# Kernel tuning notes

Measured on AMD Instinct MI355X. Metric: run time of the kernel, lower is better.

## Reference

```python
import jax, jax.numpy as jnp
import numpy as np

N_SAMPLE, N_RES = 1024, 4096

def setup_inputs() -> dict:
    key = jax.random.key(0)
    k1, k2 = jax.random.split(key)
    pred = jax.random.normal(k1, (N_SAMPLE, N_RES, 3), dtype=jnp.float32)
    true = jax.random.normal(k2, (N_RES, 3), dtype=jnp.float32)
    mask = jnp.ones((N_RES,), dtype=jnp.bool_)
    return {"pred_coordinate": pred, "true_coordinate": true, "coordinate_mask": mask}


def _tm_score(pred_coordinate, true_coordinate, coordinate_mask):
    # mask used as weights: identical to torch's boolean gather + reduce
    w = coordinate_mask.astype(jnp.float32)           # [L]
    Lt = jnp.sum(w)                                   # number of valid residues
    # d0 normalization (RNA uses protein formula), clamped at 0.5
    d0 = jnp.where(Lt <= 15.0, 0.5, 1.24 * jnp.cbrt(Lt - 15.0) - 1.8)
    d0 = jnp.maximum(d0, 0.5)
    d0_sq = d0 * d0

    wn = w / Lt                                       # normalized weights [L]
    true_mean = jnp.einsum('l,li->i', wn, true_coordinate)              # [3]
    pred_mean = jnp.einsum('l,sli->si', wn, pred_coordinate)            # [S,3]
    pred_c = pred_coordinate - pred_mean[:, None, :]                    # [S,L,3]
    true_c = true_coordinate - true_mean                                # [L,3]

    # Kabsch: covariance H_s = pred_c^T diag(w) true_c  -> [S,3,3]
    H = jnp.einsum('sli,l,lj->sij', pred_c, w, true_c)
    U, _, Vt = jnp.linalg.svd(H, full_matrices=False)
    V = jnp.swapaxes(Vt, -1, -2)
    # proper rotation (no reflection): flip sign of last singular vector if det<0
    det = jnp.linalg.det(jnp.einsum('sij,skj->sik', V, U))              # det(V U^T)
    D = jnp.stack([jnp.ones_like(det), jnp.ones_like(det), jnp.sign(det)], axis=-1)  # [S,3]
    R = jnp.einsum('sij,sj,skj->sik', V, D, U)        # R = V diag(D) U^T, [S,3,3]

    aligned = jnp.einsum('sij,slj->sli', R, pred_c) + true_mean         # [S,L,3]
    d_sq = jnp.sum((aligned - true_coordinate) ** 2, axis=-1)           # [S,L]
    terms = 1.0 / (1.0 + d_sq / d0_sq)
    tm = jnp.einsum('sl,l->s', terms, wn)             # masked mean -> [S]
    return tm


def reference(pred_coordinate, true_coordinate, coordinate_mask):
    return _tm_score(pred_coordinate, true_coordinate, coordinate_mask)
```

## Files before the change

### kernel.cpp

```cpp
#include <hip/hip_runtime.h>
#include <math.h>


#define NS        1024
#define NL        4096
#define TPB       256
#define CHUNK_RES 1024
#define NCHUNK    4

__device__ __forceinline__ float waveReduceSum(float v) {
    #pragma unroll
    for (int off = 32; off > 0; off >>= 1)
        v += __shfl_down(v, off, 64);
    return v;
}

__device__ __forceinline__ double det3(const double B[4][4],
                                       int r0, int r1, int r2,
                                       int c0, int c1, int c2) {
    return B[r0][c0]*(B[r1][c1]*B[r2][c2] - B[r1][c2]*B[r2][c1])
         - B[r0][c1]*(B[r1][c0]*B[r2][c2] - B[r1][c2]*B[r2][c0])
         + B[r0][c2]*(B[r1][c0]*B[r2][c1] - B[r1][c1]*B[r2][c0]);
}

__global__ __launch_bounds__(TPB, 4) void tm_fused(
    const float* __restrict__ pred, const float* __restrict__ tru,
    const int* __restrict__ mask, float* __restrict__ out)
{
    const int s    = blockIdx.x;
    const int tid  = threadIdx.x;
    const int wave = tid >> 6, lane = tid & 63;
    const float* ps = pred + (size_t)s * NL * 3;

    __shared__ float ldsP[CHUNK_RES * 3];
    __shared__ float ldsT[CHUNK_RES * 3];
    __shared__ float sred[4][18];

    float acc[18];
    #pragma unroll
    for (int i = 0; i < 18; ++i) acc[i] = 0.f;

    for (int k = 0; k < NCHUNK; ++k) {
        const float4* gp = (const float4*)(ps  + (size_t)k * CHUNK_RES * 3);
        const float4* gt = (const float4*)(tru + (size_t)k * CHUNK_RES * 3);
        float4* lp = (float4*)ldsP;
        float4* lt = (float4*)ldsT;
        #pragma unroll
        for (int j = 0; j < 3; ++j) {
            const int idx = wave * 192 + j * 64 + lane;
            lp[idx] = gp[idx];
            lt[idx] = gt[idx];
        }
        __syncthreads();

        const float4* rp = (const float4*)&ldsP[tid * 12];
        const float4* rt = (const float4*)&ldsT[tid * 12];
        const float4 q0 = rp[0], q1 = rp[1], q2 = rp[2];
        const float4 u0 = rt[0], u1 = rt[1], u2 = rt[2];
        const int4   mi = *(const int4*)(mask + k * CHUNK_RES + tid * 4);

        const float px[4] = {q0.x, q0.w, q1.z, q2.y};
        const float py[4] = {q0.y, q1.x, q1.w, q2.z};
        const float pz[4] = {q0.z, q1.y, q2.x, q2.w};
        const float tx[4] = {u0.x, u0.w, u1.z, u2.y};
        const float ty[4] = {u0.y, u1.x, u1.w, u2.z};
        const float tz[4] = {u0.z, u1.y, u2.x, u2.w};
        const float wm[4] = {mi.x ? 1.f : 0.f, mi.y ? 1.f : 0.f,
                             mi.z ? 1.f : 0.f, mi.w ? 1.f : 0.f};

        #pragma unroll
        for (int r = 0; r < 4; ++r) {
            const float w = wm[r];
            const float wpx = w * px[r], wpy = w * py[r], wpz = w * pz[r];
            acc[0] += w;
            acc[1] += w * tx[r]; acc[2] += w * ty[r]; acc[3] += w * tz[r];
            acc[4] += wpx; acc[5] += wpy; acc[6] += wpz;
            acc[7]  += wpx * tx[r]; acc[8]  += wpx * ty[r]; acc[9]  += wpx * tz[r];
            acc[10] += wpy * tx[r]; acc[11] += wpy * ty[r]; acc[12] += wpy * tz[r];
            acc[13] += wpz * tx[r]; acc[14] += wpz * ty[r]; acc[15] += wpz * tz[r];
            acc[16] += wpx * px[r] + wpy * py[r] + wpz * pz[r];
            acc[17] += w * (tx[r]*tx[r] + ty[r]*ty[r] + tz[r]*tz[r]);
        }
        __syncthreads();
    }

    #pragma unroll
    for (int i = 0; i < 18; ++i) {
        float r = waveReduceSum(acc[i]);
        if (lane == 0) sred[wave][i] = r;
    }
    __syncthreads();

    double S[18];
    #pragma unroll
    for (int i = 0; i < 18; ++i)
        S[i] = (double)sred[0][i] + (double)sred[1][i]
             + (double)sred[2][i] + (double)sred[3][i];

    const double Lt = S[0], invLt = 1.0 / Lt;
    const double tmxd = S[1]*invLt, tmyd = S[2]*invLt, tmzd = S[3]*invLt;
    const double pmxd = S[4]*invLt, pmyd = S[5]*invLt, pmzd = S[6]*invLt;

    double HA[3][3];
    const double Sp[3] = {S[4], S[5], S[6]};
    const double St[3] = {S[1], S[2], S[3]};
    #pragma unroll
    for (int i = 0; i < 3; ++i)
        #pragma unroll
        for (int j = 0; j < 3; ++j)
            HA[i][j] = (S[7 + i*3 + j] - Sp[i]*St[j]*invLt) * invLt;
    const double gA = (S[16] - (Sp[0]*Sp[0]+Sp[1]*Sp[1]+Sp[2]*Sp[2])*invLt) * invLt;
    const double gB = (S[17] - (St[0]*St[0]+St[1]*St[1]+St[2]*St[2])*invLt) * invLt;

    const double Sxx=HA[0][0], Sxy=HA[0][1], Sxz=HA[0][2];
    const double Syx=HA[1][0], Syy=HA[1][1], Syz=HA[1][2];
    const double Szx=HA[2][0], Szy=HA[2][1], Szz=HA[2][2];
    double K[4][4] = {
      { Sxx+Syy+Szz, Syz-Szy,      Szx-Sxz,      Sxy-Syx      },
      { Syz-Szy,     Sxx-Syy-Szz,  Sxy+Syx,      Szx+Sxz      },
      { Szx-Sxz,     Sxy+Syx,      Syy-Sxx-Szz,  Syz+Szy      },
      { Sxy-Syx,     Szx+Sxz,      Syz+Szy,      Szz-Sxx-Syy  }
    };

    double E2 = 0.0;
    #pragma unroll
    for (int i = 0; i < 4; ++i)
        #pragma unroll
        for (int j = 0; j < 4; ++j)
            if (j > i) E2 += K[i][i]*K[j][j] - K[i][j]*K[i][j];
    const double E3 = det3(K,1,2,3, 1,2,3) + det3(K,0,2,3, 0,2,3)
                    + det3(K,0,1,3, 0,1,3) + det3(K,0,1,2, 0,1,2);
    const double E4 = K[0][0]*det3(K,1,2,3, 1,2,3) - K[0][1]*det3(K,1,2,3, 0,2,3)
                    + K[0][2]*det3(K,1,2,3, 0,1,3) - K[0][3]*det3(K,1,2,3, 0,1,2);

    double lam = 0.5 * (gA + gB);
    #pragma unroll
    for (int it = 0; it < 8; ++it) {
        const double l2 = lam * lam;
        const double P  = ((l2 + E2) * lam - E3) * lam + E4;
        const double Pd = (4.0 * l2 + 2.0 * E2) * lam - E3;
        if (fabs(Pd) < 1e-300) break;
        lam -= P / Pd;
    }

    #pragma unroll
    for (int i = 0; i < 4; ++i) K[i][i] -= lam;
    double best[4] = {1.0, 0.0, 0.0, 0.0};
    double bestn = -1.0;
    #pragma unroll
    for (int r = 0; r < 4; ++r) {
        int ri[3]; int t = 0;
        #pragma unroll
        for (int i = 0; i < 4; ++i) if (i != r) ri[t++] = i;
        double v[4];
        #pragma unroll
        for (int c = 0; c < 4; ++c) {
            int cj[3]; t = 0;
            #pragma unroll
            for (int j = 0; j < 4; ++j) if (j != c) cj[t++] = j;
            const double d = det3(K, ri[0],ri[1],ri[2], cj[0],cj[1],cj[2]);
            v[c] = ((r + c) & 1) ? -d : d;
        }
        const double n = v[0]*v[0]+v[1]*v[1]+v[2]*v[2]+v[3]*v[3];
        if (n > bestn) { bestn = n; best[0]=v[0]; best[1]=v[1]; best[2]=v[2]; best[3]=v[3]; }
    }
    const double qn = 1.0 / sqrt(bestn);
    const double q0d = best[0]*qn, qxd = best[1]*qn, qyd = best[2]*qn, qzd = best[3]*qn;

    const float R00 = (float)(q0d*q0d+qxd*qxd-qyd*qyd-qzd*qzd);
    const float R01 = (float)(2.0*(qxd*qyd - q0d*qzd));
    const float R02 = (float)(2.0*(qxd*qzd + q0d*qyd));
    const float R10 = (float)(2.0*(qyd*qxd + q0d*qzd));
    const float R11 = (float)(q0d*q0d-qxd*qxd+qyd*qyd-qzd*qzd);
    const float R12 = (float)(2.0*(qyd*qzd - q0d*qxd));
    const float R20 = (float)(2.0*(qzd*qxd - q0d*qyd));
    const float R21 = (float)(2.0*(qzd*qyd + q0d*qxd));
    const float R22 = (float)(q0d*q0d-qxd*qxd-qyd*qyd+qzd*qzd);

    double d0 = (Lt <= 15.0) ? 0.5 : (1.24 * cbrt(Lt - 15.0) - 1.8);
    if (d0 < 0.5) d0 = 0.5;
    const float inv_d0sq = (float)(1.0 / (d0 * d0));
    const float invLtf   = (float)invLt;
    const float pmx = (float)pmxd, pmy = (float)pmyd, pmz = (float)pmzd;
    const float tmx = (float)tmxd, tmy = (float)tmyd, tmz = (float)tmzd;

    float tacc = 0.f;
    for (int k = 0; k < NCHUNK; ++k) {
        const float4* gp = (const float4*)(ps  + (size_t)k * CHUNK_RES * 3);
        const float4* gt = (const float4*)(tru + (size_t)k * CHUNK_RES * 3);
        float4* lp = (float4*)ldsP;
        float4* lt = (float4*)ldsT;
        #pragma unroll
        for (int j = 0; j < 3; ++j) {
            const int idx = wave * 192 + j * 64 + lane;
            lp[idx] = gp[idx];
            lt[idx] = gt[idx];
        }
        __syncthreads();

        const float4* rp = (const float4*)&ldsP[tid * 12];
        const float4* rt = (const float4*)&ldsT[tid * 12];
        const float4 q0 = rp[0], q1 = rp[1], q2 = rp[2];
        const float4 u0 = rt[0], u1 = rt[1], u2 = rt[2];
        const int4   mi = *(const int4*)(mask + k * CHUNK_RES + tid * 4);

        const float px[4] = {q0.x, q0.w, q1.z, q2.y};
        const float py[4] = {q0.y, q1.x, q1.w, q2.z};
        const float pz[4] = {q0.z, q1.y, q2.x, q2.w};
        const float tx[4] = {u0.x, u0.w, u1.z, u2.y};
        const float ty[4] = {u0.y, u1.x, u1.w, u2.z};
        const float tz[4] = {u0.z, u1.y, u2.x, u2.w};
        const float wm[4] = {mi.x ? 1.f : 0.f, mi.y ? 1.f : 0.f,
                             mi.z ? 1.f : 0.f, mi.w ? 1.f : 0.f};

        #pragma unroll
        for (int r = 0; r < 4; ++r) {
            const float vx = px[r] - pmx, vy = py[r] - pmy, vz = pz[r] - pmz;
            const float a0 = R00*vx + R01*vy + R02*vz + tmx - tx[r];
            const float a1 = R10*vx + R11*vy + R12*vz + tmy - ty[r];
            const float a2 = R20*vx + R21*vy + R22*vz + tmz - tz[r];
            const float dsq = a0*a0 + a1*a1 + a2*a2;
            tacc += wm[r] * __builtin_amdgcn_rcpf(1.0f + dsq * inv_d0sq);
        }
        __syncthreads();
    }
    tacc *= invLtf;

    float r = waveReduceSum(tacc);
    if (lane == 0) sred[wave][0] = r;
    __syncthreads();
    if (tid == 0)
        out[s] = sred[0][0] + sred[1][0] + sred[2][0] + sred[3][0];
}

extern "C" void kernel_launch(void* const* d_in, const int* in_sizes, int n_in,
                              void* d_out, int out_size, void* d_ws, size_t ws_size,
                              hipStream_t stream) {
    const float* pred = (const float*)d_in[0];
    const float* tru  = (const float*)d_in[1];
    const int*   mask = (const int*)d_in[2];
    float* out = (float*)d_out;
    (void)d_ws; (void)ws_size;
    tm_fused<<<NS, TPB, 0, stream>>>(pred, tru, mask, out);
}
```

Measured before the change: 99.17 us.

## Stage full pred sample into LDS via async global_load_lds, read true from global

```diff
diff --git a/kernel.cpp b/kernel.cpp
--- a/kernel.cpp
+++ b/kernel.cpp
@@ -5,8 +5,6 @@
 #define NS        1024
 #define NL        4096
 #define TPB       256
-#define CHUNK_RES 1024
-#define NCHUNK    4
 
 __device__ __forceinline__ float waveReduceSum(float v) {
     #pragma unroll
@@ -23,7 +21,14 @@
          + B[r0][c2]*(B[r1][c0]*B[r2][c1] - B[r1][c1]*B[r2][c0]);
 }
 
-__global__ __launch_bounds__(TPB, 4) void tm_fused(
+__device__ __forceinline__ void async_copy16(void* lds_dst, const void* g_src) {
+    __builtin_amdgcn_global_load_lds(
+        (const __attribute__((address_space(1))) void*)g_src,
+        (__attribute__((address_space(3))) void*)lds_dst,
+        16, 0, 0);
+}
+
+__global__ __launch_bounds__(TPB, 3) void tm_fused(
     const float* __restrict__ pred, const float* __restrict__ tru,
     const int* __restrict__ mask, float* __restrict__ out)
 {
@@ -32,32 +37,44 @@
     const int wave = tid >> 6, lane = tid & 63;
     const float* ps = pred + (size_t)s * NL * 3;
 
-    __shared__ float ldsP[CHUNK_RES * 3];
-    __shared__ float ldsT[CHUNK_RES * 3];
+    __shared__ float ldsP[NL * 3];
     __shared__ float sred[4][18];
+    __shared__ float sfin[4];
+
+    const float4* gp4 = (const float4*)ps;
+    float4* lp4 = (float4*)ldsP;
+    #pragma unroll
+    for (int j = 0; j < 12; ++j) {
+        const int base = wave * 768 + j * 64;
+        async_copy16((void*)(lp4 + base), (const void*)(gp4 + base + lane));
+    }
+
+    unsigned mbits = 0;
+    {
+        #pragma unroll
+        for (int k = 0; k < 4; ++k) {
+            const int4 mi = *(const int4*)(mask + k * 1024 + tid * 4);
+            if (mi.x) mbits |= 1u << (k * 4 + 0);
+            if (mi.y) mbits |= 1u << (k * 4 + 1);
+            if (mi.z) mbits |= 1u << (k * 4 + 2);
+            if (mi.w) mbits |= 1u << (k * 4 + 3);
+        }
+    }
+
+    __syncthreads();
 
     float acc[18];
     #pragma unroll
     for (int i = 0; i < 18; ++i) acc[i] = 0.f;
 
-    for (int k = 0; k < NCHUNK; ++k) {
-        const float4* gp = (const float4*)(ps  + (size_t)k * CHUNK_RES * 3);
-        const float4* gt = (const float4*)(tru + (size_t)k * CHUNK_RES * 3);
-        float4* lp = (float4*)ldsP;
-        float4* lt = (float4*)ldsT;
-        #pragma unroll
-        for (int j = 0; j < 3; ++j) {
-            const int idx = wave * 192 + j * 64 + lane;
-            lp[idx] = gp[idx];
-            lt[idx] = gt[idx];
-        }
-        __syncthreads();
-
-        const float4* rp = (const float4*)&ldsP[tid * 12];
-        const float4* rt = (const float4*)&ldsT[tid * 12];
+    const float4* gt4 = (const float4*)tru;
+    #pragma unroll
+    for (int k = 0; k < 4; ++k) {
+        const float4* rp = (const float4*)&ldsP[k * 3072 + tid * 12];
         const float4 q0 = rp[0], q1 = rp[1], q2 = rp[2];
-        const float4 u0 = rt[0], u1 = rt[1], u2 = rt[2];
-        const int4   mi = *(const int4*)(mask + k * CHUNK_RES + tid * 4);
+        const float4 u0 = gt4[k * 768 + tid * 3 + 0];
+        const float4 u1 = gt4[k * 768 + tid * 3 + 1];
+        const float4 u2 = gt4[k * 768 + tid * 3 + 2];
 
         const float px[4] = {q0.x, q0.w, q1.z, q2.y};
         const float py[4] = {q0.y, q1.x, q1.w, q2.z};
@@ -65,12 +82,10 @@
         const float tx[4] = {u0.x, u0.w, u1.z, u2.y};
         const float ty[4] = {u0.y, u1.x, u1.w, u2.z};
         const float tz[4] = {u0.z, u1.y, u2.x, u2.w};
-        const float wm[4] = {mi.x ? 1.f : 0.f, mi.y ? 1.f : 0.f,
-                             mi.z ? 1.f : 0.f, mi.w ? 1.f : 0.f};
 
         #pragma unroll
         for (int r = 0; r < 4; ++r) {
-            const float w = wm[r];
+            const float w = ((mbits >> (k * 4 + r)) & 1u) ? 1.f : 0.f;
             const float wpx = w * px[r], wpy = w * py[r], wpz = w * pz[r];
             acc[0] += w;
             acc[1] += w * tx[r]; acc[2] += w * ty[r]; acc[3] += w * tz[r];
@@ -81,7 +96,6 @@
             acc[16] += wpx * px[r] + wpy * py[r] + wpz * pz[r];
             acc[17] += w * (tx[r]*tx[r] + ty[r]*ty[r] + tz[r]*tz[r]);
         }
-        __syncthreads();
     }
 
     #pragma unroll
@@ -185,24 +199,13 @@
     const float tmx = (float)tmxd, tmy = (float)tmyd, tmz = (float)tmzd;
 
     float tacc = 0.f;
-    for (int k = 0; k < NCHUNK; ++k) {
-        const float4* gp = (const float4*)(ps  + (size_t)k * CHUNK_RES * 3);
-        const float4* gt = (const float4*)(tru + (size_t)k * CHUNK_RES * 3);
-        float4* lp = (float4*)ldsP;
-        float4* lt = (float4*)ldsT;
-        #pragma unroll
-        for (int j = 0; j < 3; ++j) {
-            const int idx = wave * 192 + j * 64 + lane;
-            lp[idx] = gp[idx];
-            lt[idx] = gt[idx];
-        }
-        __syncthreads();
-
-        const float4* rp = (const float4*)&ldsP[tid * 12];
-        const float4* rt = (const float4*)&ldsT[tid * 12];
+    #pragma unroll
+    for (int k = 0; k < 4; ++k) {
+        const float4* rp = (const float4*)&ldsP[k * 3072 + tid * 12];
         const float4 q0 = rp[0], q1 = rp[1], q2 = rp[2];
-        const float4 u0 = rt[0], u1 = rt[1], u2 = rt[2];
-        const int4   mi = *(const int4*)(mask + k * CHUNK_RES + tid * 4);
+        const float4 u0 = gt4[k * 768 + tid * 3 + 0];
+        const float4 u1 = gt4[k * 768 + tid * 3 + 1];
+        const float4 u2 = gt4[k * 768 + tid * 3 + 2];
 
         const float px[4] = {q0.x, q0.w, q1.z, q2.y};
         const float py[4] = {q0.y, q1.x, q1.w, q2.z};
@@ -210,27 +213,25 @@
         const float tx[4] = {u0.x, u0.w, u1.z, u2.y};
         const float ty[4] = {u0.y, u1.x, u1.w, u2.z};
         const float tz[4] = {u0.z, u1.y, u2.x, u2.w};
-        const float wm[4] = {mi.x ? 1.f : 0.f, mi.y ? 1.f : 0.f,
-                             mi.z ? 1.f : 0.f, mi.w ? 1.f : 0.f};
 
         #pragma unroll
         for (int r = 0; r < 4; ++r) {
+            const float w = ((mbits >> (k * 4 + r)) & 1u) ? 1.f : 0.f;
             const float vx = px[r] - pmx, vy = py[r] - pmy, vz = pz[r] - pmz;
             const float a0 = R00*vx + R01*vy + R02*vz + tmx - tx[r];
             const float a1 = R10*vx + R11*vy + R12*vz + tmy - ty[r];
             const float a2 = R20*vx + R21*vy + R22*vz + tmz - tz[r];
             const float dsq = a0*a0 + a1*a1 + a2*a2;
-            tacc += wm[r] * __builtin_amdgcn_rcpf(1.0f + dsq * inv_d0sq);
-        }
-        __syncthreads();
+            tacc += w * __builtin_amdgcn_rcpf(1.0f + dsq * inv_d0sq);
+        }
     }
     tacc *= invLtf;
 
     float r = waveReduceSum(tacc);
-    if (lane == 0) sred[wave][0] = r;
+    if (lane == 0) sfin[wave] = r;
     __syncthreads();
     if (tid == 0)
-        out[s] = sred[0][0] + sred[1][0] + sred[2][0] + sred[3][0];
+        out[s] = sfin[0] + sfin[1] + sfin[2] + sfin[3];
 }
 
 extern "C" void kernel_launch(void* const* d_in, const int* in_sizes, int n_in,
```

New measurement: 113.4 us. 1.14x slower.
